# Optimization experiments

Measured on AMD Instinct MI355X. Metric: run time of the kernel, lower is better.

The kernel has to match this reference:

```python
import jax, jax.numpy as jnp
import numpy as np

NUM_Q_HEADS = 32
NUM_KV_HEADS = 8
HEAD_DIM = 128
ROPE_THETA = 10000.0


def _apply_rope(x, positions):
    # x: (B, T, H, D) real; rotate pairs (x[2i], x[2i+1]) by angle pos * inv_freq[i]
    B, T, H, D = x.shape
    half = D // 2
    inv_freq = 1.0 / (ROPE_THETA ** (jnp.arange(half, dtype=jnp.float32) / half))
    freqs = positions.astype(jnp.float32)[:, None] * inv_freq[None, :]  # (T, half)
    cos = jnp.cos(freqs)[None, :, None, :]  # (1, T, 1, half)
    sin = jnp.sin(freqs)[None, :, None, :]
    xr = x.reshape(B, T, H, half, 2)
    x1, x2 = xr[..., 0], xr[..., 1]
    o1 = x1 * cos - x2 * sin
    o2 = x1 * sin + x2 * cos
    return jnp.stack([o1, o2], axis=-1).reshape(B, T, H, D)


def setup_inputs() -> dict:
    key = jax.random.key(0)
    ks = jax.random.split(key, 8)
    B, T, C = 2, 1024, 4096
    x = jax.random.normal(ks[0], (B, T, C), dtype=jnp.float32)
    cache_keys = jax.random.normal(ks[1], (B, 4096, NUM_KV_HEADS, HEAD_DIM), dtype=jnp.float32)
    cache_values = jax.random.normal(ks[2], (B, 4096, NUM_KV_HEADS, HEAD_DIM), dtype=jnp.float32)
    s = 0.02
    Wq = jax.random.normal(ks[3], (C, C), dtype=jnp.float32) * s
    Wk = jax.random.normal(ks[4], (NUM_KV_HEADS * HEAD_DIM, C), dtype=jnp.float32) * s
    Wv = jax.random.normal(ks[5], (NUM_KV_HEADS * HEAD_DIM, C), dtype=jnp.float32) * s
    Wo = jax.random.normal(ks[6], (C, C), dtype=jnp.float32) * s
    return {"x": x, "start_pos": 1024, "cache_keys": cache_keys,
            "cache_values": cache_values, "Wq": Wq, "Wk": Wk, "Wv": Wv, "Wo": Wo}


def reference(x, start_pos, cache_keys, cache_values, Wq, Wk, Wv, Wo):
    B, T, C = x.shape
    D = HEAD_DIM
    G = NUM_Q_HEADS // NUM_KV_HEADS  # queries per kv head
    end_pos = start_pos + T
    scale = 1.0 / np.sqrt(D).astype(np.float32)

    # QKV projections (torch Linear: y = x @ W.T)
    q = jnp.einsum('btc,oc->bto', x, Wq).reshape(B, T, NUM_Q_HEADS, D)
    k = jnp.einsum('btc,oc->bto', x, Wk).reshape(B, T, NUM_KV_HEADS, D)
    v = jnp.einsum('btc,oc->bto', x, Wv).reshape(B, T, NUM_KV_HEADS, D)

    # RoPE at absolute positions [start_pos, end_pos)
    positions = jnp.arange(start_pos, end_pos)
    q = _apply_rope(q, positions)
    k = _apply_rope(k, positions)

    # KV-cache write (detached in the original -> stop_gradient)
    cache_keys = cache_keys.at[:, start_pos:end_pos].set(jax.lax.stop_gradient(k))
    cache_values = cache_values.at[:, start_pos:end_pos].set(jax.lax.stop_gradient(v))
    k_full = jax.lax.stop_gradient(cache_keys[:, :end_pos])   # (B, S, Hkv, D)
    v_full = jax.lax.stop_gradient(cache_values[:, :end_pos])
    S = end_pos

    # GQA attention without materializing repeated K/V:
    # q heads h map to kv head h // G (repeat_interleave ordering)
    qg = q.reshape(B, T, NUM_KV_HEADS, G, D)
    scores = jnp.einsum('btkgd,bskd->bkgts', qg, k_full) * scale  # (B,Hkv,G,T,S)

    # causal mask over the cache: query i sees cache positions j <= start_pos + i
    i = jnp.arange(T)[:, None]
    j = jnp.arange(S)[None, :]
    visible = j <= (start_pos + i)  # (T, S)
    scores = jnp.where(visible[None, None, None], scores, jnp.finfo(scores.dtype).min)
    probs = jax.nn.softmax(scores, axis=-1)

    ctx = jnp.einsum('bkgts,bskd->btkgd', probs, v_full).reshape(B, T, C)
    return jnp.einsum('btc,oc->bto', ctx, Wo)
```

## Files before the change

### kernel.cpp

```cpp
#include <hip/hip_runtime.h>
#include <math.h>


typedef __bf16 bf16x8 __attribute__((ext_vector_type(8)));
typedef float floatx4 __attribute__((ext_vector_type(4)));

constexpr int SMAX = 2048;
constexpr size_t KT_OFF = (size_t)2 * 1024 * 4096;
constexpr size_t VT_OFF = KT_OFF + (size_t)2 * 8 * SMAX * 128;
constexpr size_t WS_XB = 0;
constexpr size_t WS_WQ = 8388608;
constexpr size_t WS_WK = 25165824;
constexpr size_t WS_WV = 29360128;
constexpr size_t WS_WO = 33554432;
constexpr size_t WS_FULL_BYTES = 100663296;

__device__ __forceinline__ unsigned short f2bf(float f) {
  union { float f; unsigned int u; } v; v.f = f;
  unsigned int u = v.u;
  return (unsigned short)((u + 0x7fffu + ((u >> 16) & 1u)) >> 16);
}

__device__ __forceinline__ bf16x8 pack8(float4 a, float4 b) {
  bf16x8 v;
  v[0] = (__bf16)a.x; v[1] = (__bf16)a.y; v[2] = (__bf16)a.z; v[3] = (__bf16)a.w;
  v[4] = (__bf16)b.x; v[5] = (__bf16)b.y; v[6] = (__bf16)b.z; v[7] = (__bf16)b.w;
  return v;
}

__device__ __forceinline__ void gll16(const unsigned short* g, unsigned short* l) {
  __builtin_amdgcn_global_load_lds((const __attribute__((address_space(1))) void*)g,
                                   (__attribute__((address_space(3))) void*)l, 16, 0, 0);
}

__global__ __launch_bounds__(256) void cvt_x(const float* __restrict__ x,
                                             unsigned short* __restrict__ xb) {
  for (size_t c = (size_t)blockIdx.x * 256 + threadIdx.x; c < 1048576; c += (size_t)gridDim.x * 256) {
    float4 f0 = ((const float4*)x)[c * 2], f1 = ((const float4*)x)[c * 2 + 1];
    ((bf16x8*)xb)[c] = pack8(f0, f1);
  }
}

__global__ __launch_bounds__(256) void cvt_full(const float* __restrict__ x,
                                                const float* __restrict__ wq,
                                                const float* __restrict__ wk,
                                                const float* __restrict__ wv,
                                                const float* __restrict__ wo,
                                                unsigned short* __restrict__ ws) {
  const size_t n0 = 1048576, n1 = n0 + 2097152, n2 = n1 + 524288, n3 = n2 + 524288, n4 = n3 + 2097152;
  for (size_t c = (size_t)blockIdx.x * 256 + threadIdx.x; c < n4; c += (size_t)gridDim.x * 256) {
    const float* src; unsigned short* dst; size_t off;
    if (c < n0)      { src = x;  dst = ws + WS_XB; off = c; }
    else if (c < n1) { src = wq; dst = ws + WS_WQ; off = c - n0; }
    else if (c < n2) { src = wk; dst = ws + WS_WK; off = c - n1; }
    else if (c < n3) { src = wv; dst = ws + WS_WV; off = c - n2; }
    else             { src = wo; dst = ws + WS_WO; off = c - n3; }
    float4 f0 = ((const float4*)src)[off * 2], f1 = ((const float4*)src)[off * 2 + 1];
    ((bf16x8*)dst)[off] = pack8(f0, f1);
  }
}

__global__ __launch_bounds__(256) void rope_prep(const int* __restrict__ spp,
                                                 float* __restrict__ tab) {
  int idx = blockIdx.x * 256 + threadIdx.x;
  int t = idx >> 6, i = idx & 63;
  float ang = (float)(spp[0] + t) * exp2f(-(float)i * 0.2076205059304602f);
  tab[idx] = sinf(ang);
  tab[65536 + idx] = cosf(ang);
}

__global__ __launch_bounds__(256) void convert_cache(const float* __restrict__ ck,
                                                     const float* __restrict__ cv,
                                                     const int* __restrict__ spp,
                                                     unsigned short* __restrict__ kt,
                                                     unsigned short* __restrict__ vt) {
  const int sp = spp[0];
  const int bk = blockIdx.y;
  const int b = bk >> 3, kh = bk & 7;
  const int s1 = blockIdx.x * 128;
  if (s1 >= sp) return;
  const int tid = threadIdx.x;
#pragma unroll
  for (int it = 0; it < 8; ++it) {
    int c = tid + it * 256;
    int s = c >> 4, dc = (c & 15) * 8;
    if (s1 + s < sp) {
      const float* src = ck + (((size_t)(b * 4096 + s1 + s)) * 8 + kh) * 128 + dc;
      *(bf16x8*)(kt + ((size_t)bk * SMAX + s1 + s) * 128 + dc) = pack8(*(const float4*)src, *(const float4*)(src + 4));
    }
  }
#pragma unroll
  for (int it = 0; it < 8; ++it) {
    int c = tid + it * 256;
    int d = c & 127, sg = c >> 7;
    bf16x8 tmp;
#pragma unroll
    for (int ss = 0; ss < 8; ++ss) {
      int s = s1 + sg * 8 + ss;
      tmp[ss] = (s < sp) ? (__bf16)cv[(((size_t)(b * 4096 + s)) * 8 + kh) * 128 + d] : (__bf16)0.0f;
    }
    *(bf16x8*)(vt + (size_t)bk * 128 * SMAX + (size_t)d * SMAX + s1 + sg * 8) = tmp;
  }
}

template<bool BDMA, int EPI>
__global__ __launch_bounds__(256) void gemm_core(const unsigned short* __restrict__ A,
                                                 const unsigned short* __restrict__ Bb,
                                                 const float* __restrict__ Bq,
                                                 const float* __restrict__ Bk,
                                                 const float* __restrict__ Bv,
                                                 float* __restrict__ Cout,
                                                 unsigned short* __restrict__ qb,
                                                 unsigned short* __restrict__ kt,
                                                 unsigned short* __restrict__ vt,
                                                 const float* __restrict__ tab,
                                                 const int* __restrict__ spp) {
  constexpr int SB = BDMA ? 32 : 40;
  __shared__ __align__(16) unsigned short la[128 * 32];
  __shared__ __align__(16) unsigned short lb[128 * SB];
  const int K = 4096;
  const int tid = threadIdx.x, lane = tid & 63, wv = tid >> 6;
  const int quad = lane >> 4, l16 = lane & 15;
  const int wm = (wv >> 1) * 64, wn = (wv & 1) * 64;
  const int m0 = blockIdx.y * 128, n0 = blockIdx.x * 128;
  const int sp = spp ? spp[0] : 0;

  floatx4 acc[4][4] = {};

  const int r0 = tid >> 2, kc0 = (tid & 3) * 8;
  const int r1 = (tid + 256) >> 2, kc1 = ((tid + 256) & 3) * 8;
  const unsigned short* a0 = A + (size_t)(m0 + r0) * K + kc0;
  const unsigned short* a1 = A + (size_t)(m0 + r1) * K + kc1;

  const unsigned short* bh0 = nullptr; const unsigned short* bh1 = nullptr;
  const float* bf0 = nullptr; const float* bf1 = nullptr;
  if (BDMA) {
    bh0 = Bb + (size_t)(n0 + r0) * K + kc0;
    bh1 = Bb + (size_t)(n0 + r1) * K + kc1;
  } else {
    const float* Bf; int nb;
    if (EPI == 0)      { Bf = Bq; nb = n0; }
    else {
      if (n0 < 4096)      { Bf = Bq; nb = n0; }
      else if (n0 < 5120) { Bf = Bk; nb = n0 - 4096; }
      else                { Bf = Bv; nb = n0 - 5120; }
    }
    bf0 = Bf + (size_t)(nb + r0) * K + kc0;
    bf1 = Bf + (size_t)(nb + r1) * K + kc1;
  }

  for (int k0 = 0; k0 < K; k0 += 32) {
    gll16(a0 + k0, la + tid * 8);
    gll16(a1 + k0, la + (tid + 256) * 8);
    if (BDMA) {
      gll16(bh0 + k0, lb + tid * 8);
      gll16(bh1 + k0, lb + (tid + 256) * 8);
    } else {
      bf16x8 vb0 = pack8(*(const float4*)(bf0 + k0), *(const float4*)(bf0 + k0 + 4));
      bf16x8 vb1 = pack8(*(const float4*)(bf1 + k0), *(const float4*)(bf1 + k0 + 4));
      *(bf16x8*)(lb + r0 * 40 + kc0) = vb0;
      *(bf16x8*)(lb + r1 * 40 + kc1) = vb1;
    }
    __syncthreads();
    bf16x8 af[4], bfr[4];
#pragma unroll
    for (int mi = 0; mi < 4; ++mi)
      af[mi] = *(const bf16x8*)(la + (wm + mi * 16 + l16) * 32 + quad * 8);
#pragma unroll
    for (int ni = 0; ni < 4; ++ni)
      bfr[ni] = *(const bf16x8*)(lb + (wn + ni * 16 + l16) * SB + quad * 8);
#pragma unroll
    for (int mi = 0; mi < 4; ++mi)
#pragma unroll
      for (int ni = 0; ni < 4; ++ni)
        acc[mi][ni] = __builtin_amdgcn_mfma_f32_16x16x32_bf16(af[mi], bfr[ni], acc[mi][ni], 0, 0, 0);
    __syncthreads();
  }

  if (EPI == 0) {
#pragma unroll
    for (int mi = 0; mi < 4; ++mi)
#pragma unroll
      for (int r = 0; r < 4; ++r) {
        const int row = m0 + wm + mi * 16 + quad * 4 + r;
#pragma unroll
        for (int ni = 0; ni < 4; ++ni)
          Cout[(size_t)row * 4096 + n0 + wn + ni * 16 + l16] = acc[mi][ni][r];
      }
  } else {
    const float S_L2E = 0.12751745f;
#pragma unroll
    for (int mi = 0; mi < 4; ++mi) {
#pragma unroll
      for (int r = 0; r < 4; ++r) {
        const int row = m0 + wm + mi * 16 + quad * 4 + r;
        const int b = row >> 10, t = row & 1023;
#pragma unroll
        for (int ni = 0; ni < 4; ++ni) {
          const int col = n0 + wn + ni * 16 + l16;
          float v = acc[mi][ni][r];
          if (col < 5120) {
            int dd = col & 127, i = dd >> 1;
            float sn = tab[t * 64 + i], cs = tab[65536 + t * 64 + i];
            float vp = __shfl_xor(v, 1, 64);
            float o = (dd & 1) ? (vp * sn + v * cs) : (v * cs - vp * sn);
            if (col < 4096) {
              qb[(size_t)row * 4096 + col] = f2bf(o * S_L2E);
            } else {
              int lc = col - 4096, kh = lc >> 7, d = lc & 127;
              kt[((size_t)(b * 8 + kh) * SMAX + sp + t) * 128 + d] = f2bf(o);
            }
          } else {
            int lc = col - 5120, kh = lc >> 7, d = lc & 127;
            vt[((size_t)(b * 8 + kh) * 128 + d) * SMAX + sp + t] = f2bf(v);
          }
        }
      }
    }
  }
}

__global__ __launch_bounds__(256) void attn(const unsigned short* __restrict__ qb,
                                            const unsigned short* __restrict__ ktg,
                                            const unsigned short* __restrict__ vtg,
                                            const int* __restrict__ spp,
                                            unsigned short* __restrict__ ctx) {
  __shared__ __align__(16) unsigned short kt_lds[64 * 136];
  __shared__ __align__(16) unsigned short vt_lds[128 * 72];
  __shared__ __align__(16) unsigned short p_lds[4][16 * 72];

  const int sp = spp[0];
  const int bh = blockIdx.y;
  const int b = bh >> 5, h = bh & 31;
  const int bk = b * 8 + (h >> 2);
  const int qt = (int)gridDim.x - 1 - (int)blockIdx.x;
  const int tid = threadIdx.x, lane = tid & 63, w = tid >> 6;
  const int quad = lane >> 4, l16 = lane & 15;
  const float NEG = -1e30f;

  bf16x8 qf[4];
  {
    const int qrow = qt * 64 + w * 16 + l16;
    const unsigned short* qbase = qb + ((size_t)(b * 1024 + qrow)) * 4096 + h * 128;
#pragma unroll
    for (int kk = 0; kk < 4; ++kk)
      qf[kk] = *(const bf16x8*)(qbase + kk * 32 + quad * 8);
  }

  floatx4 o[8] = {};
  float mrow[4], lrow[4];
#pragma unroll
  for (int r = 0; r < 4; ++r) { mrow[r] = NEG; lrow[r] = 0.0f; }

  const int s_end = sp + qt * 64 + 64;
  const int ntiles = (s_end + 63) >> 6;
  const unsigned short* ktb = ktg + (size_t)bk * SMAX * 128;
  const unsigned short* vtb = vtg + (size_t)bk * 128 * SMAX;

  for (int st = 0; st < ntiles; ++st) {
    const int s0 = st * 64;
#pragma unroll
    for (int it = 0; it < 4; ++it) {
      int c = tid + it * 256;
      int s = c >> 4, dc = (c & 15) * 8;
      *(bf16x8*)(kt_lds + s * 136 + dc) = *(const bf16x8*)(ktb + (size_t)(s0 + s) * 128 + dc);
    }
#pragma unroll
    for (int it = 0; it < 4; ++it) {
      int c = tid + it * 256;
      int d = c >> 3, sc = (c & 7) * 8;
      *(bf16x8*)(vt_lds + d * 72 + sc) = *(const bf16x8*)(vtb + (size_t)d * SMAX + s0 + sc);
    }
    __syncthreads();

    floatx4 sfr[4];
#pragma unroll
    for (int ni = 0; ni < 4; ++ni) {
      floatx4 a = {};
#pragma unroll
      for (int kk = 0; kk < 4; ++kk) {
        bf16x8 kf = *(const bf16x8*)(kt_lds + (ni * 16 + l16) * 136 + kk * 32 + quad * 8);
        a = __builtin_amdgcn_mfma_f32_16x16x32_bf16(qf[kk], kf, a, 0, 0, 0);
      }
      sfr[ni] = a;
    }
#pragma unroll
    for (int ni = 0; ni < 4; ++ni) {
#pragma unroll
      for (int r = 0; r < 4; ++r) {
        int j = s0 + ni * 16 + l16;
        int tg = sp + qt * 64 + w * 16 + quad * 4 + r;
        sfr[ni][r] = (j <= tg) ? sfr[ni][r] : NEG;
      }
    }
    float mnew[4], rs[4];
#pragma unroll
    for (int r = 0; r < 4; ++r) {
      float v = fmaxf(fmaxf(sfr[0][r], sfr[1][r]), fmaxf(sfr[2][r], sfr[3][r]));
#pragma unroll
      for (int off = 1; off < 16; off <<= 1) v = fmaxf(v, __shfl_xor(v, off, 64));
      mnew[r] = fmaxf(mrow[r], v);
    }
#pragma unroll
    for (int r = 0; r < 4; ++r) {
      float s = 0.0f;
#pragma unroll
      for (int ni = 0; ni < 4; ++ni) {
        float p = exp2f(sfr[ni][r] - mnew[r]);
        sfr[ni][r] = p;
        s += p;
      }
#pragma unroll
      for (int off = 1; off < 16; off <<= 1) s += __shfl_xor(s, off, 64);
      rs[r] = s;
    }
#pragma unroll
    for (int r = 0; r < 4; ++r) {
      float alpha = exp2f(mrow[r] - mnew[r]);
      lrow[r] = lrow[r] * alpha + rs[r];
      mrow[r] = mnew[r];
#pragma unroll
      for (int ni = 0; ni < 8; ++ni) o[ni][r] *= alpha;
    }
    unsigned short* pw = p_lds[w];
#pragma unroll
    for (int ni = 0; ni < 4; ++ni)
#pragma unroll
      for (int r = 0; r < 4; ++r)
        pw[(quad * 4 + r) * 72 + ni * 16 + l16] = f2bf(sfr[ni][r]);
#pragma unroll
    for (int kk = 0; kk < 2; ++kk) {
      bf16x8 pf = *(const bf16x8*)(pw + l16 * 72 + kk * 32 + quad * 8);
#pragma unroll
      for (int ni = 0; ni < 8; ++ni) {
        bf16x8 vf = *(const bf16x8*)(vt_lds + (ni * 16 + l16) * 72 + kk * 32 + quad * 8);
        o[ni] = __builtin_amdgcn_mfma_f32_16x16x32_bf16(pf, vf, o[ni], 0, 0, 0);
      }
    }
    __syncthreads();
  }

#pragma unroll
  for (int r = 0; r < 4; ++r) {
    float invl = 1.0f / lrow[r];
    int t = qt * 64 + w * 16 + quad * 4 + r;
    unsigned short* cbase = ctx + ((size_t)(b * 1024 + t)) * 4096 + h * 128;
#pragma unroll
    for (int ni = 0; ni < 8; ++ni)
      cbase[ni * 16 + l16] = f2bf(o[ni][r] * invl);
  }
}

extern "C" void kernel_launch(void* const* d_in, const int* in_sizes, int n_in,
                              void* d_out, int out_size, void* d_ws, size_t ws_size,
                              hipStream_t stream) {
  const float* x  = (const float*)d_in[0];
  const int* sp   = (const int*)d_in[1];
  float* ck       = (float*)d_in[2];
  const float* cv = (const float*)d_in[3];
  const float* Wq = (const float*)d_in[4];
  const float* Wk = (const float*)d_in[5];
  const float* Wv = (const float*)d_in[6];
  const float* Wo = (const float*)d_in[7];
  float* out      = (float*)d_out;

  unsigned short* qb  = (unsigned short*)d_out;
  unsigned short* kt  = (unsigned short*)d_out + KT_OFF;
  unsigned short* vt  = (unsigned short*)d_out + VT_OFF;
  unsigned short* ws  = (unsigned short*)d_ws;
  unsigned short* xb  = ws + WS_XB;
  unsigned short* ctx = ws + WS_XB;
  float* tab          = ck + (size_t)2048 * 1024;

  const bool full = ws_size >= WS_FULL_BYTES;

  rope_prep<<<256, 256, 0, stream>>>(sp, tab);
  convert_cache<<<dim3(16, 16), 256, 0, stream>>>(ck, cv, sp, kt, vt);

  if (full) {
    cvt_full<<<2048, 256, 0, stream>>>(x, Wq, Wk, Wv, Wo, ws);
    gemm_core<true, 1><<<dim3(48, 16), 256, 0, stream>>>(xb, ws + WS_WQ, nullptr, nullptr, nullptr,
                                                         nullptr, qb, kt, vt, tab, sp);
    attn<<<dim3(16, 64), 256, 0, stream>>>(qb, kt, vt, sp, ctx);
    gemm_core<true, 0><<<dim3(32, 16), 256, 0, stream>>>(ctx, ws + WS_WO, nullptr, nullptr, nullptr,
                                                         out, nullptr, nullptr, nullptr, nullptr, nullptr);
  } else {
    cvt_x<<<2048, 256, 0, stream>>>(x, xb);
    gemm_core<false, 1><<<dim3(48, 16), 256, 0, stream>>>(xb, nullptr, Wq, Wk, Wv,
                                                          nullptr, qb, kt, vt, tab, sp);
    attn<<<dim3(16, 64), 256, 0, stream>>>(qb, kt, vt, sp, ctx);
    gemm_core<false, 0><<<dim3(32, 16), 256, 0, stream>>>(ctx, nullptr, Wo, nullptr, nullptr,
                                                          out, nullptr, nullptr, nullptr, nullptr, nullptr);
  }
}
```

Measured before the change: 704.2 us.

## Rewrite attention kernel with 32x32 MFMA, double-buffered swizzled LDS, balanced causal pairing

Rewrites the flash-attention kernel to use 512-thread blocks whose eight waves each own 32 query rows. Waves are split between a near-diagonal and a far-from-diagonal query tile so causal work evens out across blocks. The kernel uses 32x32x16 bf16 MFMA with K-by-Q operand order, so probabilities pass between lanes by shuffles instead of LDS. K/V tiles are prefetched into registers and double-buffered in XOR-swizzled LDS. The kernel also skips fully masked subtiles, defers softmax rescaling with a lazy threshold, remaps blocks for cache locality, and stages output through LDS for coalesced stores. This adds register pressure and more complex indexing.

```diff
diff --git a/kernel.cpp b/kernel.cpp
--- a/kernel.cpp
+++ b/kernel.cpp
@@ -4,6 +4,7 @@
 
 typedef __bf16 bf16x8 __attribute__((ext_vector_type(8)));
 typedef float floatx4 __attribute__((ext_vector_type(4)));
+typedef float floatx16 __attribute__((ext_vector_type(16)));
 
 constexpr int SMAX = 2048;
 constexpr size_t KT_OFF = (size_t)2 * 1024 * 4096;
@@ -26,6 +27,12 @@
   v[0] = (__bf16)a.x; v[1] = (__bf16)a.y; v[2] = (__bf16)a.z; v[3] = (__bf16)a.w;
   v[4] = (__bf16)b.x; v[5] = (__bf16)b.y; v[6] = (__bf16)b.z; v[7] = (__bf16)b.w;
   return v;
+}
+
+__device__ __forceinline__ unsigned cvtpk_bf16(float lo, float hi) {
+  unsigned r;
+  asm("v_cvt_pk_bf16_f32 %0, %1, %2" : "=v"(r) : "v"(lo), "v"(hi));
+  return r;
 }
 
 __device__ __forceinline__ void gll16(const unsigned short* g, unsigned short* l) {
@@ -220,134 +227,163 @@
   }
 }
 
-__global__ __launch_bounds__(256) void attn(const unsigned short* __restrict__ qb,
-                                            const unsigned short* __restrict__ ktg,
-                                            const unsigned short* __restrict__ vtg,
-                                            const int* __restrict__ spp,
-                                            unsigned short* __restrict__ ctx) {
-  __shared__ __align__(16) unsigned short kt_lds[64 * 136];
-  __shared__ __align__(16) unsigned short vt_lds[128 * 72];
-  __shared__ __align__(16) unsigned short p_lds[4][16 * 72];
+__global__ __launch_bounds__(512, 2) void attn(const unsigned short* __restrict__ qb,
+                                               const unsigned short* __restrict__ ktg,
+                                               const unsigned short* __restrict__ vtg,
+                                               const int* __restrict__ spp,
+                                               unsigned short* __restrict__ ctx) {
+  __shared__ __align__(16) unsigned short lds[32768];
 
   const int sp = spp[0];
-  const int bh = blockIdx.y;
+  const int iblk = (int)blockIdx.y * 4 + (int)blockIdx.x;
+  const int lblk = (iblk & 7) * 32 + (iblk >> 3);
+  const int x = lblk & 3, bh = lblk >> 2;
   const int b = bh >> 5, h = bh & 31;
   const int bk = b * 8 + (h >> 2);
-  const int qt = (int)gridDim.x - 1 - (int)blockIdx.x;
   const int tid = threadIdx.x, lane = tid & 63, w = tid >> 6;
-  const int quad = lane >> 4, l16 = lane & 15;
-  const float NEG = -1e30f;
-
-  bf16x8 qf[4];
-  {
-    const int qrow = qt * 64 + w * 16 + l16;
-    const unsigned short* qbase = qb + ((size_t)(b * 1024 + qrow)) * 4096 + h * 128;
-#pragma unroll
-    for (int kk = 0; kk < 4; ++kk)
-      qf[kk] = *(const bf16x8*)(qbase + kk * 32 + quad * 8);
-  }
-
-  floatx4 o[8] = {};
-  float mrow[4], lrow[4];
-#pragma unroll
-  for (int r = 0; r < 4; ++r) { mrow[r] = NEG; lrow[r] = 0.0f; }
-
-  const int s_end = sp + qt * 64 + 64;
-  const int ntiles = (s_end + 63) >> 6;
+  const int hi = lane >> 5, l31 = lane & 31;
+  const int tq128 = (w < 4) ? x : (7 - x);
+  const int wq0 = tq128 * 128 + (w & 3) * 32;
+  const int q = wq0 + l31;
+  const int lim = sp + q;
+  const int wlim = sp + wq0 + 31;
+  const int nt = (sp + (8 - x) * 128 + 63) >> 6;
+
   const unsigned short* ktb = ktg + (size_t)bk * SMAX * 128;
   const unsigned short* vtb = vtg + (size_t)bk * 128 * SMAX;
 
-  for (int st = 0; st < ntiles; ++st) {
+  const int kr0 = tid >> 4, kc = tid & 15, kr1 = kr0 + 32;
+  const int ksl0 = ((kc ^ (kr0 & 15)) << 3), ksl1 = ((kc ^ (kr1 & 15)) << 3);
+  const int vd0 = tid >> 3, vc = tid & 7, vd1 = vd0 + 64;
+  const int vsl0 = ((vc ^ (vd0 & 7)) << 3), vsl1 = ((vc ^ (vd1 & 7)) << 3);
+
+  bf16x8 qf[8];
+  {
+    const unsigned short* qbase = qb + ((size_t)(b * 1024 + q)) * 4096 + h * 128 + hi * 8;
+#pragma unroll
+    for (int kg = 0; kg < 8; ++kg) qf[kg] = *(const bf16x8*)(qbase + kg * 16);
+  }
+
+  floatx16 oacc[4] = {};
+  float mrun = -1e30f, lrun = 0.0f;
+
+  *(bf16x8*)(lds + kr0 * 128 + ksl0)         = *(const bf16x8*)(ktb + (size_t)kr0 * 128 + kc * 8);
+  *(bf16x8*)(lds + kr1 * 128 + ksl1)         = *(const bf16x8*)(ktb + (size_t)kr1 * 128 + kc * 8);
+  *(bf16x8*)(lds + 16384 + vd0 * 64 + vsl0)  = *(const bf16x8*)(vtb + (size_t)vd0 * SMAX + vc * 8);
+  *(bf16x8*)(lds + 16384 + vd1 * 64 + vsl1)  = *(const bf16x8*)(vtb + (size_t)vd1 * SMAX + vc * 8);
+  __syncthreads();
+
+  int off = 0;
+  for (int st = 0; st < nt; ++st) {
     const int s0 = st * 64;
-#pragma unroll
-    for (int it = 0; it < 4; ++it) {
-      int c = tid + it * 256;
-      int s = c >> 4, dc = (c & 15) * 8;
-      *(bf16x8*)(kt_lds + s * 136 + dc) = *(const bf16x8*)(ktb + (size_t)(s0 + s) * 128 + dc);
-    }
-#pragma unroll
-    for (int it = 0; it < 4; ++it) {
-      int c = tid + it * 256;
-      int d = c >> 3, sc = (c & 7) * 8;
-      *(bf16x8*)(vt_lds + d * 72 + sc) = *(const bf16x8*)(vtb + (size_t)d * SMAX + s0 + sc);
+    bf16x8 nk0, nk1, nv0, nv1;
+    const bool pre = (st + 1 < nt);
+    if (pre) {
+      const int s1 = s0 + 64;
+      nk0 = *(const bf16x8*)(ktb + (size_t)(s1 + kr0) * 128 + kc * 8);
+      nk1 = *(const bf16x8*)(ktb + (size_t)(s1 + kr1) * 128 + kc * 8);
+      nv0 = *(const bf16x8*)(vtb + (size_t)vd0 * SMAX + s1 + vc * 8);
+      nv1 = *(const bf16x8*)(vtb + (size_t)vd1 * SMAX + s1 + vc * 8);
+      asm volatile("" ::: "memory");
+    }
+    const unsigned short* kl = lds + off;
+    const unsigned short* vl = lds + 16384 + off;
+    if (s0 <= wlim) {
+#pragma unroll
+      for (int sub = 0; sub < 2; ++sub) {
+        const int ss = s0 + sub * 32;
+        if (ss <= wlim) {
+          floatx16 sa = {0,0,0,0,0,0,0,0,0,0,0,0,0,0,0,0};
+          const unsigned short* kbase = kl + (sub * 32 + l31) * 128;
+          const int kx = l31 & 15;
+#pragma unroll
+          for (int kg = 0; kg < 8; ++kg) {
+            bf16x8 kf = *(const bf16x8*)(kbase + (((kg * 2 + hi) ^ kx) << 3));
+            sa = __builtin_amdgcn_mfma_f32_32x32x16_bf16(kf, qf[kg], sa, 0, 0, 0);
+          }
+          if (ss + 31 > sp + wq0) {
+#pragma unroll
+            for (int r = 0; r < 16; ++r) {
+              const int j = ss + (r & 3) + 8 * (r >> 2) + 4 * hi;
+              if (j > lim) sa[r] = -1e30f;
+            }
+          }
+          float mt = sa[0];
+#pragma unroll
+          for (int r = 1; r < 16; ++r) mt = fmaxf(mt, sa[r]);
+          mt = fmaxf(mt, __shfl_xor(mt, 32, 64));
+          if (!__all(mt <= mrun + 8.0f)) {
+            const float mnew = fmaxf(mrun, mt);
+            const float al = exp2f(mrun - mnew);
+#pragma unroll
+            for (int db = 0; db < 4; ++db)
+#pragma unroll
+              for (int r = 0; r < 16; ++r) oacc[db][r] *= al;
+            lrun *= al;
+            mrun = mnew;
+          }
+          float p[16]; float ls = 0.0f;
+#pragma unroll
+          for (int r = 0; r < 16; ++r) { p[r] = exp2f(sa[r] - mrun); ls += p[r]; }
+          lrun += ls + __shfl_xor(ls, 32, 64);
+#pragma unroll
+          for (int ks = 0; ks < 2; ++ks) {
+            const int rb = ks * 8;
+            unsigned a0 = cvtpk_bf16(p[rb + 0], p[rb + 1]);
+            unsigned a1 = cvtpk_bf16(p[rb + 2], p[rb + 3]);
+            unsigned b0 = cvtpk_bf16(p[rb + 4], p[rb + 5]);
+            unsigned b1 = cvtpk_bf16(p[rb + 6], p[rb + 7]);
+            const unsigned t0 = __shfl_xor(a0, 32, 64);
+            const unsigned t1 = __shfl_xor(b0, 32, 64);
+            const unsigned t2 = __shfl_xor(a1, 32, 64);
+            const unsigned t3 = __shfl_xor(b1, 32, 64);
+            union { unsigned u[4]; bf16x8 v; } pf;
+            pf.u[0] = hi ? t1 : a0;
+            pf.u[1] = hi ? t3 : a1;
+            pf.u[2] = hi ? b0 : t0;
+            pf.u[3] = hi ? b1 : t2;
+            const int sslot = sub * 4 + ks * 2 + hi;
+#pragma unroll
+            for (int db = 0; db < 4; ++db) {
+              const int vrow = db * 32 + l31;
+              bf16x8 vf = *(const bf16x8*)(vl + vrow * 64 + ((sslot ^ (l31 & 7)) << 3));
+              oacc[db] = __builtin_amdgcn_mfma_f32_32x32x16_bf16(vf, pf.v, oacc[db], 0, 0, 0);
+            }
+          }
+        }
+      }
+    }
+    if (pre) {
+      unsigned short* kn = lds + (off ^ 8192);
+      unsigned short* vn = lds + 16384 + (off ^ 8192);
+      *(bf16x8*)(kn + kr0 * 128 + ksl0) = nk0;
+      *(bf16x8*)(kn + kr1 * 128 + ksl1) = nk1;
+      *(bf16x8*)(vn + vd0 * 64 + vsl0) = nv0;
+      *(bf16x8*)(vn + vd1 * 64 + vsl1) = nv1;
     }
     __syncthreads();
-
-    floatx4 sfr[4];
-#pragma unroll
-    for (int ni = 0; ni < 4; ++ni) {
-      floatx4 a = {};
-#pragma unroll
-      for (int kk = 0; kk < 4; ++kk) {
-        bf16x8 kf = *(const bf16x8*)(kt_lds + (ni * 16 + l16) * 136 + kk * 32 + quad * 8);
-        a = __builtin_amdgcn_mfma_f32_16x16x32_bf16(qf[kk], kf, a, 0, 0, 0);
-      }
-      sfr[ni] = a;
-    }
-#pragma unroll
-    for (int ni = 0; ni < 4; ++ni) {
-#pragma unroll
-      for (int r = 0; r < 4; ++r) {
-        int j = s0 + ni * 16 + l16;
-        int tg = sp + qt * 64 + w * 16 + quad * 4 + r;
-        sfr[ni][r] = (j <= tg) ? sfr[ni][r] : NEG;
-      }
-    }
-    float mnew[4], rs[4];
-#pragma unroll
-    for (int r = 0; r < 4; ++r) {
-      float v = fmaxf(fmaxf(sfr[0][r], sfr[1][r]), fmaxf(sfr[2][r], sfr[3][r]));
-#pragma unroll
-      for (int off = 1; off < 16; off <<= 1) v = fmaxf(v, __shfl_xor(v, off, 64));
-      mnew[r] = fmaxf(mrow[r], v);
-    }
-#pragma unroll
-    for (int r = 0; r < 4; ++r) {
-      float s = 0.0f;
-#pragma unroll
-      for (int ni = 0; ni < 4; ++ni) {
-        float p = exp2f(sfr[ni][r] - mnew[r]);
-        sfr[ni][r] = p;
-        s += p;
-      }
-#pragma unroll
-      for (int off = 1; off < 16; off <<= 1) s += __shfl_xor(s, off, 64);
-      rs[r] = s;
-    }
-#pragma unroll
-    for (int r = 0; r < 4; ++r) {
-      float alpha = exp2f(mrow[r] - mnew[r]);
-      lrow[r] = lrow[r] * alpha + rs[r];
-      mrow[r] = mnew[r];
-#pragma unroll
-      for (int ni = 0; ni < 8; ++ni) o[ni][r] *= alpha;
-    }
-    unsigned short* pw = p_lds[w];
-#pragma unroll
-    for (int ni = 0; ni < 4; ++ni)
-#pragma unroll
-      for (int r = 0; r < 4; ++r)
-        pw[(quad * 4 + r) * 72 + ni * 16 + l16] = f2bf(sfr[ni][r]);
-#pragma unroll
-    for (int kk = 0; kk < 2; ++kk) {
-      bf16x8 pf = *(const bf16x8*)(pw + l16 * 72 + kk * 32 + quad * 8);
-#pragma unroll
-      for (int ni = 0; ni < 8; ++ni) {
-        bf16x8 vf = *(const bf16x8*)(vt_lds + (ni * 16 + l16) * 72 + kk * 32 + quad * 8);
-        o[ni] = __builtin_amdgcn_mfma_f32_16x16x32_bf16(pf, vf, o[ni], 0, 0, 0);
-      }
-    }
-    __syncthreads();
-  }
-
-#pragma unroll
-  for (int r = 0; r < 4; ++r) {
-    float invl = 1.0f / lrow[r];
-    int t = qt * 64 + w * 16 + quad * 4 + r;
-    unsigned short* cbase = ctx + ((size_t)(b * 1024 + t)) * 4096 + h * 128;
-#pragma unroll
-    for (int ni = 0; ni < 8; ++ni)
-      cbase[ni * 16 + l16] = f2bf(o[ni][r] * invl);
+    off ^= 8192;
+  }
+
+  const float invl = 1.0f / lrun;
+  unsigned short* myo = lds + w * 4096;
+#pragma unroll
+  for (int db = 0; db < 4; ++db)
+#pragma unroll
+    for (int i2 = 0; i2 < 8; ++i2) {
+      const int r = i2 * 2;
+      const int d = db * 32 + (r & 3) + 8 * (r >> 2) + 4 * hi;
+      const unsigned wo = cvtpk_bf16(oacc[db][r] * invl, oacc[db][r + 1] * invl);
+      *(unsigned*)(myo + l31 * 128 + (((2 * d) ^ ((l31 & 15) << 4)) >> 1)) = wo;
+    }
+  __syncthreads();
+#pragma unroll
+  for (int it = 0; it < 8; ++it) {
+    const int c = tid + it * 512;
+    const int wr = c >> 9, row = (c >> 4) & 31, c16 = c & 15;
+    const int tq = (((wr < 4) ? x : (7 - x)) * 128) + (wr & 3) * 32 + row;
+    bf16x8 vv = *(const bf16x8*)(lds + wr * 4096 + row * 128 + ((c16 ^ (row & 15)) << 3));
+    *(bf16x8*)(ctx + ((size_t)(b * 1024 + tq)) * 4096 + h * 128 + c16 * 8) = vv;
   }
 }
 
@@ -381,14 +417,14 @@
     cvt_full<<<2048, 256, 0, stream>>>(x, Wq, Wk, Wv, Wo, ws);
     gemm_core<true, 1><<<dim3(48, 16), 256, 0, stream>>>(xb, ws + WS_WQ, nullptr, nullptr, nullptr,
                                                          nullptr, qb, kt, vt, tab, sp);
-    attn<<<dim3(16, 64), 256, 0, stream>>>(qb, kt, vt, sp, ctx);
+    attn<<<dim3(4, 64), 512, 0, stream>>>(qb, kt, vt, sp, ctx);
     gemm_core<true, 0><<<dim3(32, 16), 256, 0, stream>>>(ctx, ws + WS_WO, nullptr, nullptr, nullptr,
                                                          out, nullptr, nullptr, nullptr, nullptr, nullptr);
   } else {
     cvt_x<<<2048, 256, 0, stream>>>(x, xb);
     gemm_core<false, 1><<<dim3(48, 16), 256, 0, stream>>>(xb, nullptr, Wq, Wk, Wv,
                                                           nullptr, qb, kt, vt, tab, sp);
-    attn<<<dim3(16, 64), 256, 0, stream>>>(qb, kt, vt, sp, ctx);
+    attn<<<dim3(4, 64), 512, 0, stream>>>(qb, kt, vt, sp, ctx);
     gemm_core<false, 0><<<dim3(32, 16), 256, 0, stream>>>(ctx, nullptr, Wo, nullptr, nullptr,
                                                           out, nullptr, nullptr, nullptr, nullptr, nullptr);
   }
```

Result: faster. 593.2 us (-15.8%).
